# Performance work log

Hardware: AMD Instinct MI355X
Metric: run time of the kernel (lower is better)

## Reference

```python
import jax, jax.numpy as jnp
import numpy as np

N, E, R, F, HD = 4096, 2048, 4, 128, 256
DEG_EPS = 1e-8
BN_EPS = 1e-5
LN_EPS = 1e-5


def _xavier(k, shape):
    scale = np.sqrt(2.0 / (shape[-2] + shape[-1])).astype(np.float32)
    return jax.random.normal(k, shape, jnp.float32) * scale


def setup_inputs() -> dict:
    key = jax.random.key(0)
    ks = jax.random.split(key, 8)
    X = jax.random.normal(ks[0], (N, F), jnp.float32)
    # sparse binary incidence matrices, one per relation type, stacked [R,N,E]
    H = (jax.random.uniform(ks[1], (R, N, E)) < 0.05).astype(jnp.float32)
    return {
        "X": X,
        "H": H,
        "W1": _xavier(ks[2], (R, F, HD)),
        "W2": _xavier(ks[3], (R, HD, HD)),
        "W3": _xavier(ks[4], (R, HD, F)),
        "imp": jnp.ones((3, R), jnp.float32),        # relation_importance per conv layer
        "b1": jnp.zeros((HD,), jnp.float32),
        "b2": jnp.zeros((HD,), jnp.float32),
        "b3": jnp.zeros((F,), jnp.float32),
        "bn_gamma": jnp.ones((2, HD), jnp.float32),
        "bn_beta": jnp.zeros((2, HD), jnp.float32),
        "ln_gamma": jnp.ones((2, HD), jnp.float32),
        "ln_beta": jnp.zeros((2, HD), jnp.float32),
        "rel_attn": jnp.ones((R,), jnp.float32) / R,
    }


def typed_conv(X, Hw, W, imp, bias):
    # Hw: [R,N,E] weighted incidence; theta = Dv^{-1/2} H De^{-1/2} via row/col scaling
    dv = jnp.power(Hw.sum(axis=2) + DEG_EPS, -0.5)   # [R,N]
    de = jnp.power(Hw.sum(axis=1) + DEG_EPS, -0.5)   # [R,E]
    theta = Hw * dv[:, :, None] * de[:, None, :]     # [R,N,E]
    # (theta @ theta^T) @ X computed as theta @ (theta^T @ X) -- same math, no NxN
    t = jnp.einsum('rne,nf->ref', theta, X)          # [R,E,Fin]
    Hn = jnp.einsum('rne,ref->rnf', theta, t)        # [R,N,Fin]
    out = jnp.einsum('rnf,rfo->rno', Hn, W)          # [R,N,Fout]
    out = out * jax.nn.sigmoid(imp)[:, None, None]
    return out.sum(axis=0) + bias


def bn_ln_elu(X, bg, bb, lg, lb):
    # BatchNorm1d with batch statistics (biased var), then LayerNorm, then ELU
    mu = X.mean(axis=0)
    var = X.var(axis=0)
    X = (X - mu) * jax.lax.rsqrt(var + BN_EPS) * bg + bb
    m = X.mean(axis=-1, keepdims=True)
    v = X.var(axis=-1, keepdims=True)
    X = (X - m) * jax.lax.rsqrt(v + LN_EPS) * lg + lb
    return jax.nn.elu(X)


def reference(X, H, W1, W2, W3, imp, b1, b2, b3, bn_gamma, bn_beta, ln_gamma, ln_beta, rel_attn):
    rw = jax.nn.softmax(rel_attn)
    Hw = H * rw[:, None, None]                       # weighted incidence per relation
    h = typed_conv(X, Hw, W1, imp[0], b1)
    h = bn_ln_elu(h, bn_gamma[0], bn_beta[0], ln_gamma[0], ln_beta[0])
    h = typed_conv(h, Hw, W2, imp[1], b2)
    h = bn_ln_elu(h, bn_gamma[1], bn_beta[1], ln_gamma[1], ln_beta[1])
    out = typed_conv(h, Hw, W3, imp[2], b3)
    return out + X  # residual: out_channels == in_channels by construction
```

## Files before the change

kernel.cpp:

```cpp
#include <hip/hip_runtime.h>
#include <hip/hip_bf16.h>

#define NN 4096
#define EE 2048
#define RR 4
#define FF 128
#define HDD 256

typedef __attribute__((ext_vector_type(4))) float floatx4;
typedef __attribute__((ext_vector_type(8))) __bf16 bf16x8;

#define AS1 __attribute__((address_space(1)))
#define AS3 __attribute__((address_space(3)))

__device__ __forceinline__ void async16(const void* g, void* l) {
  __builtin_amdgcn_global_load_lds((const AS1 void*)(unsigned long long)(g),
                                   (AS3 void*)(unsigned int)(unsigned long long)(l),
                                   16, 0, 0);
}

__device__ inline unsigned short f2b(float x) {
  unsigned int u = __float_as_uint(x);
  unsigned int r = u + 0x7fffu + ((u >> 16) & 1u);
  return (unsigned short)(r >> 16);
}
__device__ inline float b2f(unsigned short u) { return __uint_as_float((unsigned int)u << 16); }

__device__ inline float rel_w(const float* rel, int r) {
  float m = fmaxf(fmaxf(rel[0], rel[1]), fmaxf(rel[2], rel[3]));
  float s = 0.f;
#pragma unroll
  for (int i = 0; i < RR; i++) s += expf(rel[i] - m);
  return expf(rel[r] - m) / s;
}

__global__ void k_prep1(const float* __restrict__ H, const float* __restrict__ rel,
                        const float* __restrict__ W1, const float* __restrict__ W2,
                        const float* __restrict__ W3, const float* __restrict__ imp,
                        float* __restrict__ dvs, unsigned long long* __restrict__ mask,
                        unsigned short* __restrict__ W1catT, unsigned short* __restrict__ W2T,
                        unsigned short* __restrict__ W3T, float* __restrict__ de, float* __restrict__ cs) {
  int b = blockIdx.x;
  if (b < 4096) {
    int wave = (b << 2) | (threadIdx.x >> 6);
    int lane = threadIdx.x & 63;
    int r = wave >> 12;
    const float* row = H + (size_t)wave * EE;
    unsigned long long* mrow = mask + (size_t)wave * (EE / 64);
    float s = 0.f;
    for (int j = 0; j < EE / 64; j++) {
      float h = row[j * 64 + lane];
      s += h;
      unsigned long long m = __ballot(h != 0.0f);
      if (lane == 0) mrow[j] = m;
    }
    for (int off = 32; off; off >>= 1) s += __shfl_down(s, off);
    if (lane == 0) {
      float rwr = rel_w(rel, r);
      dvs[wave] = rwr * rsqrtf(rwr * s + 1e-8f);
    }
  } else if (b < 4096 + 2048) {
    int idx = (b - 4096) * 256 + threadIdx.x;
    if (idx < RR * FF * HDD) {
      int o = idx % HDD, f = (idx / HDD) % FF, r = idx / (HDD * FF);
      float sg = 1.0f / (1.0f + expf(-imp[r]));
      W1catT[(size_t)o * (RR * FF) + r * FF + f] = f2b(sg * W1[((size_t)r * FF + f) * HDD + o]);
    } else if (idx < RR * FF * HDD + RR * HDD * HDD) {
      int j = idx - RR * FF * HDD;
      int c = j % HDD, o = (j / HDD) % HDD, r = j / (HDD * HDD);
      float sg = 1.0f / (1.0f + expf(-imp[RR + r]));
      W2T[j] = f2b(sg * W2[((size_t)r * HDD + c) * HDD + o]);
    } else {
      int j = idx - RR * FF * HDD - RR * HDD * HDD;
      int c = j % HDD, o = (j / HDD) % FF, r = j / (HDD * FF);
      float sg = 1.0f / (1.0f + expf(-imp[2 * RR + r]));
      W3T[j] = f2b(sg * W3[((size_t)r * HDD + c) * FF + o]);
    }
  } else {
    int i = (b - 6144) * 256 + threadIdx.x;
    if (i < RR * EE) de[i] = 0.f;
    else if (i < RR * EE + 2 * HDD) cs[i - RR * EE] = 0.f;
  }
}

__global__ void k_prep2(const unsigned long long* __restrict__ m1, unsigned long long* __restrict__ m2,
                        float* __restrict__ de, const float* __restrict__ X,
                        const float* __restrict__ dvs, unsigned short* __restrict__ XdvT) {
  __shared__ unsigned long long w[64 * 33];
  __shared__ unsigned short tile[64][65];
  int t = threadIdx.x;
  if (blockIdx.x < 256) {
    int r = blockIdx.x >> 6;
    int n0 = (blockIdx.x & 63) << 6;
    const unsigned long long* src = m1 + ((size_t)r * NN + n0) * 32;
#pragma unroll
    for (int i = 0; i < 8; i++) {
      int idx = t + i * 256;
      int n = idx >> 5, W = idx & 31;
      w[n * 33 + W] = src[idx];
    }
    __syncthreads();
    int wid = t >> 6, lane = t & 63;
    int v = n0 >> 6;
#pragma unroll
    for (int Wi = 0; Wi < 8; Wi++) {
      int W = wid * 8 + Wi;
      unsigned long long myw = w[lane * 33 + W];
      unsigned long long out = 0;
      for (int b = 0; b < 64; b++) {
        unsigned long long mm = __ballot(((myw >> b) & 1ULL) != 0);
        if (lane == b) out = mm;
      }
      m2[((size_t)r * EE + W * 64 + lane) * 64 + v] = out;
      atomicAdd(&de[r * EE + W * 64 + lane], (float)__popcll(out));
    }
  } else {
    int idx = blockIdx.x - 256;
    int c0 = (idx & 1) * 64, m0 = ((idx >> 1) & 63) * 64, r = idx >> 7;
    int tr = t >> 4, tc = t & 15;
#pragma unroll
    for (int i = 0; i < 4; i++) {
      int m = m0 + tr + 16 * i;
      float d = dvs[(size_t)r * NN + m];
      float4 v = *(const float4*)(X + (size_t)m * FF + c0 + tc * 4);
      tile[tr + 16 * i][tc * 4 + 0] = f2b(v.x * d);
      tile[tr + 16 * i][tc * 4 + 1] = f2b(v.y * d);
      tile[tr + 16 * i][tc * 4 + 2] = f2b(v.z * d);
      tile[tr + 16 * i][tc * 4 + 3] = f2b(v.w * d);
    }
    __syncthreads();
    unsigned short* db = XdvT + (size_t)r * FF * NN;
#pragma unroll
    for (int i = 0; i < 4; i++) {
      int c = c0 + tr + 16 * i;
      ushort4 v;
      v.x = tile[tc * 4 + 0][tr + 16 * i];
      v.y = tile[tc * 4 + 1][tr + 16 * i];
      v.z = tile[tc * 4 + 2][tr + 16 * i];
      v.w = tile[tc * 4 + 3][tr + 16 * i];
      *(ushort4*)(db + (size_t)c * NN + m0 + tc * 4) = v;
    }
  }
}

template <int DEC, int FLAT>
__global__ __launch_bounds__(256) void k_gemm3(
    const unsigned short* __restrict__ A, const unsigned short* __restrict__ BT,
    int K, int SK, int lda, int ldb, long a_rs, long b_rs,
    unsigned short* __restrict__ P, long c_ps, long c_rs, int ldc,
    const unsigned long long* __restrict__ dm, int dnw, long drow_rs,
    const float* __restrict__ dvs_,
    const float* __restrict__ cscale, long cs_rs,
    const float* __restrict__ derow, const float* __restrict__ decol,
    const float* __restrict__ rel) {
  __shared__ unsigned short Al[2][128 * 64];
  __shared__ unsigned short Bl[2][128 * 64];
  int tid = threadIdx.x, wid = tid >> 6, lane = tid & 63;
  int m0 = blockIdx.x << 7, n0 = blockIdx.y << 7;
  int z = blockIdx.z, zr = z / SK, kz = z - zr * SK;
  int Kc = K / SK;
  int r8 = lane >> 3, c8 = lane & 7;
  int swz = ((c8 ^ r8) << 3);
  const unsigned short* Ab = A + (DEC == 1 ? 0 : ((size_t)zr * a_rs + (size_t)m0 * lda + (size_t)kz * Kc));
  const unsigned short* Bb = BT + (DEC == 2 ? 0 : ((size_t)zr * b_rs + (size_t)n0 * ldb + (size_t)kz * Kc));
  const unsigned int* mrow = nullptr;
  int drow = 0, dhalf = 0, dsw = 0;
  unsigned long long dvpack = 0;
  if (DEC) {
    drow = tid >> 1; dhalf = tid & 1;
    dsw = drow & 7;
    if (FLAT) {
      int n = m0 + drow;
#pragma unroll
      for (int r4 = 0; r4 < 4; r4++)
        dvpack |= (unsigned long long)f2b(dvs_[(r4 << 12) + n]) << (r4 << 4);
    } else {
      long mrowOff = (long)zr * drow_rs + (DEC == 1 ? m0 : n0) + drow;
      mrow = (const unsigned int*)(dm + (size_t)mrowOff * dnw);
    }
  }
  auto stage = [&](int pb, int k0) {
    if (DEC != 1) {
#pragma unroll
      for (int t = 0; t < 4; t++) {
        int rbase = (wid << 5) + (t << 3);
        int row = rbase + r8;
        async16(Ab + (size_t)row * lda + k0 + swz, &Al[pb][rbase * 64 + lane * 8]);
      }
    }
    if (DEC != 2) {
#pragma unroll
      for (int t = 0; t < 4; t++) {
        int rbase = (wid << 5) + (t << 3);
        int row = rbase + r8;
        async16(Bb + (size_t)row * ldb + k0 + swz, &Bl[pb][rbase * 64 + lane * 8]);
      }
    }
    if (DEC) {
      unsigned short* Dl = (DEC == 1) ? &Al[pb][0] : &Bl[pb][0];
      long kglob = (long)kz * Kc + k0;
      unsigned int bits;
      unsigned short sval;
      if (FLAT) {
        int rr = (int)(kglob >> 11);
        int ew = (((int)kglob) & 2047) >> 5;
        bits = ((const unsigned int*)dm)[(((size_t)rr << 12) + (size_t)(m0 + drow)) * 64 + ew + dhalf];
        sval = (unsigned short)(dvpack >> ((rr & 3) << 4));
      } else {
        bits = mrow[(kglob >> 5) + dhalf];
        sval = (unsigned short)0x3F80;
      }
      uint4 zz = {0u, 0u, 0u, 0u};
#pragma unroll
      for (int g = 0; g < 4; g++) {
        int chunk = ((dhalf << 2) | g) ^ dsw;
        *(uint4*)&Dl[drow * 64 + chunk * 8] = zz;
      }
      while (bits) {
        int b = __builtin_ctz(bits);
        bits &= bits - 1;
        int kl = (dhalf << 5) + b;
        Dl[drow * 64 + (((kl >> 3) ^ dsw) << 3) + (kl & 7)] = sval;
      }
    }
  };
  int wm = (wid >> 1) << 6, wn = (wid & 1) << 6;
  int fm = lane & 15, quad = lane >> 4;
  int f7 = fm & 7;
  floatx4 acc[4][4];
#pragma unroll
  for (int i = 0; i < 4; i++)
#pragma unroll
    for (int j = 0; j < 4; j++) acc[i][j] = (floatx4){0.f, 0.f, 0.f, 0.f};
  auto compute = [&](int pb) {
#pragma unroll
    for (int ks = 0; ks < 2; ks++) {
      int kg = (ks << 2) | quad;
      int ko = ((kg ^ f7) << 3);
      bf16x8 a[4], b[4];
#pragma unroll
      for (int i = 0; i < 4; i++) {
        a[i] = *(const bf16x8*)&Al[pb][(wm + i * 16 + fm) * 64 + ko];
        b[i] = *(const bf16x8*)&Bl[pb][(wn + i * 16 + fm) * 64 + ko];
      }
#pragma unroll
      for (int i = 0; i < 4; i++)
#pragma unroll
        for (int j = 0; j < 4; j++)
          acc[i][j] = __builtin_amdgcn_mfma_f32_16x16x32_bf16(a[i], b[j], acc[i][j], 0, 0, 0);
    }
  };
  stage(0, 0);
  __syncthreads();
  for (int k0 = 0; k0 < Kc; k0 += 128) {
    if (k0 + 64 < Kc) stage(1, k0 + 64);
    compute(0);
    __syncthreads();
    if (k0 + 128 < Kc) stage(0, k0 + 128);
    compute(1);
    __syncthreads();
  }
  unsigned short* Cb = P + (size_t)kz * c_ps + (size_t)zr * c_rs;
  float rwr = (derow || decol) ? rel_w(rel, zr) : 0.f;
  float csc[4];
#pragma unroll
  for (int ni = 0; ni < 4; ni++) {
    int col = n0 + wn + ni * 16 + fm;
    float c = 1.0f;
    if (cscale) c = cscale[(size_t)zr * cs_rs + col];
    if (decol) c = 1.0f / (rwr * decol[(size_t)zr * EE + col] + 1e-8f);
    csc[ni] = c;
  }
#pragma unroll
  for (int mi = 0; mi < 4; mi++)
#pragma unroll
    for (int ni = 0; ni < 4; ni++)
#pragma unroll
      for (int v = 0; v < 4; v++) {
        int row = m0 + wm + mi * 16 + quad * 4 + v;
        int col = n0 + wn + ni * 16 + fm;
        float val = acc[mi][ni][v] * csc[ni];
        if (derow) val *= 1.0f / (rwr * derow[(size_t)zr * EE + row] + 1e-8f);
        Cb[(size_t)row * ldc + col] = f2b(val);
      }
}

__global__ void k_red_b(const unsigned short* __restrict__ P, unsigned short* __restrict__ out,
                        int SK, long region, float* __restrict__ cszero) {
  if (cszero && blockIdx.x == 0 && blockIdx.y == 0) {
    cszero[threadIdx.x] = 0.f;
    cszero[threadIdx.x + 256] = 0.f;
  }
  long i = ((long)blockIdx.x * 256 + threadIdx.x) * 8;
  int zr = blockIdx.y;
  const unsigned short* p = P + (size_t)zr * SK * region + i;
  float s[8] = {0, 0, 0, 0, 0, 0, 0, 0};
  for (int k = 0; k < SK; k++) {
    const unsigned short* q = p + (size_t)k * region;
    ushort4 a = *(const ushort4*)q;
    ushort4 b = *(const ushort4*)(q + 4);
    s[0] += b2f(a.x); s[1] += b2f(a.y); s[2] += b2f(a.z); s[3] += b2f(a.w);
    s[4] += b2f(b.x); s[5] += b2f(b.y); s[6] += b2f(b.z); s[7] += b2f(b.w);
  }
  ushort4 o0, o1;
  o0.x = f2b(s[0]); o0.y = f2b(s[1]); o0.z = f2b(s[2]); o0.w = f2b(s[3]);
  o1.x = f2b(s[4]); o1.y = f2b(s[5]); o1.z = f2b(s[6]); o1.w = f2b(s[7]);
  unsigned short* d = out + (size_t)zr * region + i;
  *(ushort4*)d = o0;
  *(ushort4*)(d + 4) = o1;
}

__global__ void k_redstats(const unsigned short* __restrict__ P, float* __restrict__ out,
                           float* __restrict__ cs, float* __restrict__ cs2, int Z) {
  __shared__ float sm[2][8][256];
  int cg = (threadIdx.x & 31) << 3;
  int rowt = threadIdx.x >> 5;
  int r0 = blockIdx.x * 32;
  float s[8] = {0, 0, 0, 0, 0, 0, 0, 0}, s2[8] = {0, 0, 0, 0, 0, 0, 0, 0};
  for (int j = 0; j < 4; j++) {
    int row = r0 + rowt * 4 + j;
    long idx = (long)row * HDD + cg;
    float acc[8] = {0, 0, 0, 0, 0, 0, 0, 0};
    for (int z = 0; z < Z; z++) {
      const unsigned short* p = P + (size_t)z * ((long)NN * HDD) + idx;
      ushort4 a = *(const ushort4*)p;
      ushort4 b = *(const ushort4*)(p + 4);
      acc[0] += b2f(a.x); acc[1] += b2f(a.y); acc[2] += b2f(a.z); acc[3] += b2f(a.w);
      acc[4] += b2f(b.x); acc[5] += b2f(b.y); acc[6] += b2f(b.z); acc[7] += b2f(b.w);
    }
    float4 o0 = {acc[0], acc[1], acc[2], acc[3]};
    float4 o1 = {acc[4], acc[5], acc[6], acc[7]};
    *(float4*)(out + idx) = o0;
    *(float4*)(out + idx + 4) = o1;
#pragma unroll
    for (int i = 0; i < 8; i++) { s[i] += acc[i]; s2[i] += acc[i] * acc[i]; }
  }
#pragma unroll
  for (int i = 0; i < 8; i++) { sm[0][rowt][cg + i] = s[i]; sm[1][rowt][cg + i] = s2[i]; }
  __syncthreads();
  int c = threadIdx.x;
  float a0 = 0, a1 = 0;
#pragma unroll
  for (int t = 0; t < 8; t++) { a0 += sm[0][t][c]; a1 += sm[1][t][c]; }
  atomicAdd(&cs[c], a0);
  atomicAdd(&cs2[c], a1);
}

__global__ void k_red_out(const unsigned short* __restrict__ P, const float* __restrict__ X,
                          const float* __restrict__ b3, float* __restrict__ out, int Z) {
  long i = ((long)blockIdx.x * 256 + threadIdx.x) * 4;
  int f = (int)(i & 127);
  float4 s = *(const float4*)(X + i);
  s.x += b3[f]; s.y += b3[f + 1]; s.z += b3[f + 2]; s.w += b3[f + 3];
  for (int z = 0; z < Z; z++) {
    ushort4 v = *(const ushort4*)(P + (size_t)z * (NN * FF) + i);
    s.x += b2f(v.x); s.y += b2f(v.y); s.z += b2f(v.z); s.w += b2f(v.w);
  }
  *(float4*)(out + i) = s;
}

__global__ void k_bnlnelu(const float* __restrict__ x, const float* __restrict__ cs, const float* __restrict__ cs2,
                          const float* __restrict__ bg, const float* __restrict__ bb,
                          const float* __restrict__ lg, const float* __restrict__ lb,
                          unsigned short* __restrict__ out) {
  int wid = threadIdx.x >> 6, lane = threadIdx.x & 63;
  int n = blockIdx.x * 4 + wid;
  float y[4];
  float m = 0.f;
#pragma unroll
  for (int j = 0; j < 4; j++) {
    int c = lane + 64 * j;
    float mu = cs[c] * (1.0f / NN);
    float var = cs2[c] * (1.0f / NN) - mu * mu;
    float xv = x[(size_t)n * HDD + c];
    y[j] = (xv - mu) * rsqrtf(var + 1e-5f) * bg[c] + bb[c];
    m += y[j];
  }
  for (int off = 32; off; off >>= 1) m += __shfl_down(m, off);
  m = __shfl(m, 0) * (1.0f / HDD);
  float var = 0.f;
#pragma unroll
  for (int j = 0; j < 4; j++) { float d = y[j] - m; var += d * d; }
  for (int off = 32; off; off >>= 1) var += __shfl_down(var, off);
  var = __shfl(var, 0) * (1.0f / HDD);
  float inv = rsqrtf(var + 1e-5f);
#pragma unroll
  for (int j = 0; j < 4; j++) {
    int c = lane + 64 * j;
    float z = (y[j] - m) * inv * lg[c] + lb[c];
    z = z > 0.f ? z : expm1f(z);
    out[(size_t)n * HDD + c] = f2b(z);
  }
}

extern "C" void kernel_launch(void* const* d_in, const int* in_sizes, int n_in,
                              void* d_out, int out_size, void* d_ws, size_t ws_size,
                              hipStream_t stream) {
  const float* X   = (const float*)d_in[0];
  const float* H   = (const float*)d_in[1];
  const float* W1  = (const float*)d_in[2];
  const float* W2  = (const float*)d_in[3];
  const float* W3  = (const float*)d_in[4];
  const float* imp = (const float*)d_in[5];
  const float* b3  = (const float*)d_in[8];
  const float* bng = (const float*)d_in[9];
  const float* bnb = (const float*)d_in[10];
  const float* lng = (const float*)d_in[11];
  const float* lnb = (const float*)d_in[12];
  const float* rel = (const float*)d_in[13];
  (void)in_sizes; (void)n_in; (void)out_size; (void)ws_size;

  char* w = (char*)d_ws;
  size_t off = 0;
  auto alloc = [&](size_t bytes) -> void* {
    void* p = w + off;
    off += (bytes + 255) & ~(size_t)255;
    return p;
  };
  float* dvs  = (float*)alloc((size_t)RR * NN * 4);
  float* de   = (float*)alloc((size_t)RR * EE * 4);
  float* cs   = (float*)alloc(2 * HDD * 4);
  unsigned long long* mask1 = (unsigned long long*)alloc((size_t)RR * NN * (EE / 64) * 8);
  unsigned long long* mask2 = (unsigned long long*)alloc((size_t)RR * EE * (NN / 64) * 8);
  unsigned short* bufP = (unsigned short*)alloc((size_t)16 * NN * HDD * 2);
  unsigned short* bufC = (unsigned short*)alloc((size_t)RR * EE * HDD * 2);
  unsigned short* bufD = (unsigned short*)alloc((size_t)RR * EE * HDD * 2);
  unsigned short* bufE = (unsigned short*)alloc((size_t)RR * EE * HDD * 2);
  float* convout = (float*)alloc((size_t)NN * HDD * 4);
  unsigned short* Xb    = (unsigned short*)alloc((size_t)NN * HDD * 2);
  unsigned short* XdvT  = (unsigned short*)alloc((size_t)RR * FF * NN * 2);
  unsigned short* hwdvT = (unsigned short*)alloc((size_t)RR * HDD * NN * 2);
  unsigned short* W1catT = (unsigned short*)alloc((size_t)RR * FF * HDD * 2);
  unsigned short* W2T    = (unsigned short*)alloc((size_t)RR * HDD * HDD * 2);
  unsigned short* W3T    = (unsigned short*)alloc((size_t)RR * HDD * FF * 2);
  unsigned short* Z1T  = bufD;
  unsigned short* bufE2 = bufE;
  unsigned short* ydvT = XdvT;
  unsigned short* bufC2 = bufC;

  k_prep1<<<4096 + 2048 + 34, 256, 0, stream>>>(H, rel, W1, W2, W3, imp,
                                                dvs, mask1, W1catT, W2T, W3T, de, cs);
  k_prep2<<<256 + 512, 256, 0, stream>>>(mask1, mask2, de, X, dvs, XdvT);

  k_gemm3<1, 0><<<dim3(EE / 128, 1, RR * 8), 256, 0, stream>>>(
      nullptr, XdvT, NN, 8, 0, NN, 0, (long)FF * NN,
      bufP, (long)EE * FF, 8L * EE * FF, FF,
      mask2, NN / 64, EE, nullptr, nullptr, 0, de, nullptr, rel);
  k_red_b<<<dim3((EE * FF) / 2048, RR), 256, 0, stream>>>(bufP, bufC, 8, (long)EE * FF, nullptr);
  k_gemm3<0, 0><<<dim3(HDD / 128, EE / 128, RR), 256, 0, stream>>>(
      W1catT, bufC, FF, 1, RR * FF, FF, FF, (long)EE * FF,
      Z1T, 0, EE, RR * EE,
      nullptr, 0, 0, nullptr, nullptr, 0, nullptr, nullptr, nullptr);
  k_gemm3<1, 1><<<dim3(NN / 128, HDD / 128, 8), 256, 0, stream>>>(
      nullptr, Z1T, RR * EE, 8, 0, RR * EE, 0, 0,
      bufP, (long)NN * HDD, 0, HDD,
      mask1, 0, 0, dvs, nullptr, 0, nullptr, nullptr, nullptr);
  k_redstats<<<NN / 32, 256, 0, stream>>>(bufP, convout, cs, cs + HDD, 8);
  k_bnlnelu<<<NN / 4, 256, 0, stream>>>(convout, cs, cs + HDD, bng, bnb, lng, lnb, Xb);

  k_gemm3<0, 0><<<dim3(HDD / 128, NN / 128, RR), 256, 0, stream>>>(
      W2T, Xb, HDD, 1, HDD, HDD, (long)HDD * HDD, 0,
      hwdvT, 0, (long)HDD * NN, NN,
      nullptr, 0, 0, nullptr, dvs, NN, nullptr, nullptr, nullptr);
  k_gemm3<2, 0><<<dim3(HDD / 128, EE / 128, RR * 4), 256, 0, stream>>>(
      hwdvT, nullptr, NN, 4, NN, 0, (long)HDD * NN, 0,
      bufP, (long)HDD * RR * EE, EE, RR * EE,
      mask2, NN / 64, EE, nullptr, nullptr, 0, nullptr, de, rel);
  k_red_b<<<dim3((HDD * RR * EE) / 2048, 1), 256, 0, stream>>>(
      bufP, bufE2, 4, (long)HDD * RR * EE, cs);
  k_gemm3<1, 1><<<dim3(NN / 128, HDD / 128, 8), 256, 0, stream>>>(
      nullptr, bufE2, RR * EE, 8, 0, RR * EE, 0, 0,
      bufP, (long)NN * HDD, 0, HDD,
      mask1, 0, 0, dvs, nullptr, 0, nullptr, nullptr, nullptr);
  k_redstats<<<NN / 32, 256, 0, stream>>>(bufP, convout, cs, cs + HDD, 8);
  k_bnlnelu<<<NN / 4, 256, 0, stream>>>(convout, cs, cs + HDD, bng + HDD, bnb + HDD, lng + HDD, lnb + HDD, Xb);

  k_gemm3<0, 0><<<dim3(1, NN / 128, RR), 256, 0, stream>>>(
      W3T, Xb, HDD, 1, HDD, HDD, (long)FF * HDD, 0,
      ydvT, 0, (long)FF * NN, NN,
      nullptr, 0, 0, nullptr, dvs, NN, nullptr, nullptr, nullptr);
  k_gemm3<2, 0><<<dim3(1, EE / 128, RR * 8), 256, 0, stream>>>(
      ydvT, nullptr, NN, 8, NN, 0, (long)FF * NN, 0,
      bufP, (long)FF * RR * EE, EE, RR * EE,
      mask2, NN / 64, EE, nullptr, nullptr, 0, nullptr, de, rel);
  k_red_b<<<dim3((FF * RR * EE) / 2048, 1), 256, 0, stream>>>(
      bufP, bufC2, 8, (long)FF * RR * EE, nullptr);
  k_gemm3<1, 1><<<dim3(NN / 128, 1, 16), 256, 0, stream>>>(
      nullptr, bufC2, RR * EE, 16, 0, RR * EE, 0, 0,
      bufP, (long)NN * FF, 0, FF,
      mask1, 0, 0, dvs, nullptr, 0, nullptr, nullptr, nullptr);
  k_red_out<<<(NN * FF) / 1024, 256, 0, stream>>>(bufP, X, b3, (float*)d_out, 16);
}
```

Baseline: 490.6 us.

## Replace dense decoded-mask GEMMs with bitmask sparse gather-sum kernels

Drops the dense GEMMs that expanded the binary incidence masks into bf16 tiles and multiplied them on the matrix cores. In their place come wave-per-row sparse kernels that walk the bitmask with readlane/ctz, gather rows of the transformed features, and accumulate them in fp32. This removes split-K partial buffers and their reduction kernels, and folds the degree scaling, the residual add and the output into the gather kernels. Feature layouts change from transposed to row-major to suit the gathers. At about 5% density this skips most of the zero work, but it trades dense MFMA throughput for irregular, latency-bound memory gathers with serial dependencies.

```diff
diff --git a/kernel.cpp b/kernel.cpp
--- a/kernel.cpp
+++ b/kernel.cpp
@@ -24,7 +24,6 @@
   unsigned int r = u + 0x7fffu + ((u >> 16) & 1u);
   return (unsigned short)(r >> 16);
 }
-__device__ inline float b2f(unsigned short u) { return __uint_as_float((unsigned int)u << 16); }
 
 __device__ inline float rel_w(const float* rel, int r) {
   float m = fmaxf(fmaxf(rel[0], rel[1]), fmaxf(rel[2], rel[3]));
@@ -39,7 +38,8 @@
                         const float* __restrict__ W3, const float* __restrict__ imp,
                         float* __restrict__ dvs, unsigned long long* __restrict__ mask,
                         unsigned short* __restrict__ W1catT, unsigned short* __restrict__ W2T,
-                        unsigned short* __restrict__ W3T, float* __restrict__ de, float* __restrict__ cs) {
+                        unsigned short* __restrict__ W3T, float* __restrict__ de,
+                        float* __restrict__ csbuf) {
   int b = blockIdx.x;
   if (b < 4096) {
     int wave = (b << 2) | (threadIdx.x >> 6);
@@ -79,15 +79,14 @@
   } else {
     int i = (b - 6144) * 256 + threadIdx.x;
     if (i < RR * EE) de[i] = 0.f;
-    else if (i < RR * EE + 2 * HDD) cs[i - RR * EE] = 0.f;
+    else if (i < RR * EE + 8 * 512) csbuf[i - RR * EE] = 0.f;
   }
 }
 
 __global__ void k_prep2(const unsigned long long* __restrict__ m1, unsigned long long* __restrict__ m2,
                         float* __restrict__ de, const float* __restrict__ X,
-                        const float* __restrict__ dvs, unsigned short* __restrict__ XdvT) {
+                        const float* __restrict__ dvs, unsigned short* __restrict__ Xdv) {
   __shared__ unsigned long long w[64 * 33];
-  __shared__ unsigned short tile[64][65];
   int t = threadIdx.x;
   if (blockIdx.x < 256) {
     int r = blockIdx.x >> 6;
@@ -115,113 +114,42 @@
       atomicAdd(&de[r * EE + W * 64 + lane], (float)__popcll(out));
     }
   } else {
-    int idx = blockIdx.x - 256;
-    int c0 = (idx & 1) * 64, m0 = ((idx >> 1) & 63) * 64, r = idx >> 7;
-    int tr = t >> 4, tc = t & 15;
-#pragma unroll
-    for (int i = 0; i < 4; i++) {
-      int m = m0 + tr + 16 * i;
-      float d = dvs[(size_t)r * NN + m];
-      float4 v = *(const float4*)(X + (size_t)m * FF + c0 + tc * 4);
-      tile[tr + 16 * i][tc * 4 + 0] = f2b(v.x * d);
-      tile[tr + 16 * i][tc * 4 + 1] = f2b(v.y * d);
-      tile[tr + 16 * i][tc * 4 + 2] = f2b(v.z * d);
-      tile[tr + 16 * i][tc * 4 + 3] = f2b(v.w * d);
-    }
-    __syncthreads();
-    unsigned short* db = XdvT + (size_t)r * FF * NN;
-#pragma unroll
-    for (int i = 0; i < 4; i++) {
-      int c = c0 + tr + 16 * i;
-      ushort4 v;
-      v.x = tile[tc * 4 + 0][tr + 16 * i];
-      v.y = tile[tc * 4 + 1][tr + 16 * i];
-      v.z = tile[tc * 4 + 2][tr + 16 * i];
-      v.w = tile[tc * 4 + 3][tr + 16 * i];
-      *(ushort4*)(db + (size_t)c * NN + m0 + tc * 4) = v;
-    }
-  }
-}
-
-template <int DEC, int FLAT>
+    int g = (blockIdx.x - 256) * 256 + t;
+    int f8 = g & 15, n = (g >> 4) & (NN - 1), r = g >> 16;
+    const float* xp = X + (size_t)n * FF + (f8 << 3);
+    float4 v0 = *(const float4*)xp;
+    float4 v1 = *(const float4*)(xp + 4);
+    float d = dvs[(r << 12) + n];
+    ushort4 o0, o1;
+    o0.x = f2b(v0.x * d); o0.y = f2b(v0.y * d); o0.z = f2b(v0.z * d); o0.w = f2b(v0.w * d);
+    o1.x = f2b(v1.x * d); o1.y = f2b(v1.y * d); o1.z = f2b(v1.z * d); o1.w = f2b(v1.w * d);
+    unsigned short* dp = Xdv + ((size_t)r * NN + n) * FF + (f8 << 3);
+    *(ushort4*)dp = o0;
+    *(ushort4*)(dp + 4) = o1;
+  }
+}
+
 __global__ __launch_bounds__(256) void k_gemm3(
     const unsigned short* __restrict__ A, const unsigned short* __restrict__ BT,
-    int K, int SK, int lda, int ldb, long a_rs, long b_rs,
-    unsigned short* __restrict__ P, long c_ps, long c_rs, int ldc,
-    const unsigned long long* __restrict__ dm, int dnw, long drow_rs,
-    const float* __restrict__ dvs_,
-    const float* __restrict__ cscale, long cs_rs,
-    const float* __restrict__ derow, const float* __restrict__ decol,
-    const float* __restrict__ rel) {
+    int K, int lda, int ldb, long a_rs, long b_rs,
+    unsigned short* __restrict__ P, long c_rs, int ldc,
+    const float* __restrict__ rscale, long rs_rs) {
   __shared__ unsigned short Al[2][128 * 64];
   __shared__ unsigned short Bl[2][128 * 64];
   int tid = threadIdx.x, wid = tid >> 6, lane = tid & 63;
   int m0 = blockIdx.x << 7, n0 = blockIdx.y << 7;
-  int z = blockIdx.z, zr = z / SK, kz = z - zr * SK;
-  int Kc = K / SK;
+  int zr = blockIdx.z;
   int r8 = lane >> 3, c8 = lane & 7;
   int swz = ((c8 ^ r8) << 3);
-  const unsigned short* Ab = A + (DEC == 1 ? 0 : ((size_t)zr * a_rs + (size_t)m0 * lda + (size_t)kz * Kc));
-  const unsigned short* Bb = BT + (DEC == 2 ? 0 : ((size_t)zr * b_rs + (size_t)n0 * ldb + (size_t)kz * Kc));
-  const unsigned int* mrow = nullptr;
-  int drow = 0, dhalf = 0, dsw = 0;
-  unsigned long long dvpack = 0;
-  if (DEC) {
-    drow = tid >> 1; dhalf = tid & 1;
-    dsw = drow & 7;
-    if (FLAT) {
-      int n = m0 + drow;
-#pragma unroll
-      for (int r4 = 0; r4 < 4; r4++)
-        dvpack |= (unsigned long long)f2b(dvs_[(r4 << 12) + n]) << (r4 << 4);
-    } else {
-      long mrowOff = (long)zr * drow_rs + (DEC == 1 ? m0 : n0) + drow;
-      mrow = (const unsigned int*)(dm + (size_t)mrowOff * dnw);
-    }
-  }
+  const unsigned short* Ab = A + (size_t)zr * a_rs + (size_t)m0 * lda;
+  const unsigned short* Bb = BT + (size_t)zr * b_rs + (size_t)n0 * ldb;
   auto stage = [&](int pb, int k0) {
-    if (DEC != 1) {
-#pragma unroll
-      for (int t = 0; t < 4; t++) {
-        int rbase = (wid << 5) + (t << 3);
-        int row = rbase + r8;
-        async16(Ab + (size_t)row * lda + k0 + swz, &Al[pb][rbase * 64 + lane * 8]);
-      }
-    }
-    if (DEC != 2) {
-#pragma unroll
-      for (int t = 0; t < 4; t++) {
-        int rbase = (wid << 5) + (t << 3);
-        int row = rbase + r8;
-        async16(Bb + (size_t)row * ldb + k0 + swz, &Bl[pb][rbase * 64 + lane * 8]);
-      }
-    }
-    if (DEC) {
-      unsigned short* Dl = (DEC == 1) ? &Al[pb][0] : &Bl[pb][0];
-      long kglob = (long)kz * Kc + k0;
-      unsigned int bits;
-      unsigned short sval;
-      if (FLAT) {
-        int rr = (int)(kglob >> 11);
-        int ew = (((int)kglob) & 2047) >> 5;
-        bits = ((const unsigned int*)dm)[(((size_t)rr << 12) + (size_t)(m0 + drow)) * 64 + ew + dhalf];
-        sval = (unsigned short)(dvpack >> ((rr & 3) << 4));
-      } else {
-        bits = mrow[(kglob >> 5) + dhalf];
-        sval = (unsigned short)0x3F80;
-      }
-      uint4 zz = {0u, 0u, 0u, 0u};
-#pragma unroll
-      for (int g = 0; g < 4; g++) {
-        int chunk = ((dhalf << 2) | g) ^ dsw;
-        *(uint4*)&Dl[drow * 64 + chunk * 8] = zz;
-      }
-      while (bits) {
-        int b = __builtin_ctz(bits);
-        bits &= bits - 1;
-        int kl = (dhalf << 5) + b;
-        Dl[drow * 64 + (((kl >> 3) ^ dsw) << 3) + (kl & 7)] = sval;
-      }
+#pragma unroll
+    for (int t = 0; t < 4; t++) {
+      int rbase = (wid << 5) + (t << 3);
+      int row = rbase + r8;
+      async16(Ab + (size_t)row * lda + k0 + swz, &Al[pb][rbase * 64 + lane * 8]);
+      async16(Bb + (size_t)row * ldb + k0 + swz, &Bl[pb][rbase * 64 + lane * 8]);
     }
   };
   int wm = (wid >> 1) << 6, wn = (wid & 1) << 6;
@@ -252,114 +180,236 @@
   };
   stage(0, 0);
   __syncthreads();
-  for (int k0 = 0; k0 < Kc; k0 += 128) {
-    if (k0 + 64 < Kc) stage(1, k0 + 64);
+  for (int k0 = 0; k0 < K; k0 += 128) {
+    if (k0 + 64 < K) stage(1, k0 + 64);
     compute(0);
     __syncthreads();
-    if (k0 + 128 < Kc) stage(0, k0 + 128);
+    if (k0 + 128 < K) stage(0, k0 + 128);
     compute(1);
     __syncthreads();
   }
-  unsigned short* Cb = P + (size_t)kz * c_ps + (size_t)zr * c_rs;
-  float rwr = (derow || decol) ? rel_w(rel, zr) : 0.f;
-  float csc[4];
-#pragma unroll
-  for (int ni = 0; ni < 4; ni++) {
-    int col = n0 + wn + ni * 16 + fm;
-    float c = 1.0f;
-    if (cscale) c = cscale[(size_t)zr * cs_rs + col];
-    if (decol) c = 1.0f / (rwr * decol[(size_t)zr * EE + col] + 1e-8f);
-    csc[ni] = c;
-  }
+  unsigned short* Cb = P + (size_t)zr * c_rs;
 #pragma unroll
   for (int mi = 0; mi < 4; mi++)
 #pragma unroll
-    for (int ni = 0; ni < 4; ni++)
-#pragma unroll
-      for (int v = 0; v < 4; v++) {
-        int row = m0 + wm + mi * 16 + quad * 4 + v;
+    for (int v = 0; v < 4; v++) {
+      int row = m0 + wm + mi * 16 + quad * 4 + v;
+      float rs = rscale ? rscale[(size_t)zr * rs_rs + row] : 1.0f;
+#pragma unroll
+      for (int ni = 0; ni < 4; ni++) {
         int col = n0 + wn + ni * 16 + fm;
-        float val = acc[mi][ni][v] * csc[ni];
-        if (derow) val *= 1.0f / (rwr * derow[(size_t)zr * EE + row] + 1e-8f);
-        Cb[(size_t)row * ldc + col] = f2b(val);
-      }
-}
-
-__global__ void k_red_b(const unsigned short* __restrict__ P, unsigned short* __restrict__ out,
-                        int SK, long region, float* __restrict__ cszero) {
-  if (cszero && blockIdx.x == 0 && blockIdx.y == 0) {
-    cszero[threadIdx.x] = 0.f;
-    cszero[threadIdx.x + 256] = 0.f;
-  }
-  long i = ((long)blockIdx.x * 256 + threadIdx.x) * 8;
-  int zr = blockIdx.y;
-  const unsigned short* p = P + (size_t)zr * SK * region + i;
-  float s[8] = {0, 0, 0, 0, 0, 0, 0, 0};
-  for (int k = 0; k < SK; k++) {
-    const unsigned short* q = p + (size_t)k * region;
-    ushort4 a = *(const ushort4*)q;
-    ushort4 b = *(const ushort4*)(q + 4);
-    s[0] += b2f(a.x); s[1] += b2f(a.y); s[2] += b2f(a.z); s[3] += b2f(a.w);
-    s[4] += b2f(b.x); s[5] += b2f(b.y); s[6] += b2f(b.z); s[7] += b2f(b.w);
-  }
-  ushort4 o0, o1;
-  o0.x = f2b(s[0]); o0.y = f2b(s[1]); o0.z = f2b(s[2]); o0.w = f2b(s[3]);
-  o1.x = f2b(s[4]); o1.y = f2b(s[5]); o1.z = f2b(s[6]); o1.w = f2b(s[7]);
-  unsigned short* d = out + (size_t)zr * region + i;
-  *(ushort4*)d = o0;
-  *(ushort4*)(d + 4) = o1;
-}
-
-__global__ void k_redstats(const unsigned short* __restrict__ P, float* __restrict__ out,
-                           float* __restrict__ cs, float* __restrict__ cs2, int Z) {
-  __shared__ float sm[2][8][256];
-  int cg = (threadIdx.x & 31) << 3;
-  int rowt = threadIdx.x >> 5;
-  int r0 = blockIdx.x * 32;
-  float s[8] = {0, 0, 0, 0, 0, 0, 0, 0}, s2[8] = {0, 0, 0, 0, 0, 0, 0, 0};
-  for (int j = 0; j < 4; j++) {
-    int row = r0 + rowt * 4 + j;
-    long idx = (long)row * HDD + cg;
-    float acc[8] = {0, 0, 0, 0, 0, 0, 0, 0};
-    for (int z = 0; z < Z; z++) {
-      const unsigned short* p = P + (size_t)z * ((long)NN * HDD) + idx;
-      ushort4 a = *(const ushort4*)p;
-      ushort4 b = *(const ushort4*)(p + 4);
-      acc[0] += b2f(a.x); acc[1] += b2f(a.y); acc[2] += b2f(a.z); acc[3] += b2f(a.w);
-      acc[4] += b2f(b.x); acc[5] += b2f(b.y); acc[6] += b2f(b.z); acc[7] += b2f(b.w);
-    }
-    float4 o0 = {acc[0], acc[1], acc[2], acc[3]};
-    float4 o1 = {acc[4], acc[5], acc[6], acc[7]};
-    *(float4*)(out + idx) = o0;
-    *(float4*)(out + idx + 4) = o1;
-#pragma unroll
-    for (int i = 0; i < 8; i++) { s[i] += acc[i]; s2[i] += acc[i] * acc[i]; }
-  }
-#pragma unroll
-  for (int i = 0; i < 8; i++) { sm[0][rowt][cg + i] = s[i]; sm[1][rowt][cg + i] = s2[i]; }
+        Cb[(size_t)row * ldc + col] = f2b(acc[mi][ni][v] * rs);
+      }
+    }
+}
+
+template <int C>
+__global__ __launch_bounds__(256) void k_b2s(
+    const unsigned long long* __restrict__ mask2, const unsigned short* __restrict__ T,
+    const float* __restrict__ de, const float* __restrict__ rel,
+    unsigned short* __restrict__ out, float* __restrict__ csz) {
+  if (blockIdx.x == 0) {
+#pragma unroll
+    for (int i = 0; i < 16; i++) csz[i * 256 + threadIdx.x] = 0.f;
+  }
+  int wv = (blockIdx.x << 2) | (threadIdx.x >> 6);
+  int lane = threadIdx.x & 63;
+  int r = wv >> 11, e = wv & (EE - 1);
+  unsigned long long w = mask2[(size_t)wv * 64 + lane];
+  unsigned int wlo = (unsigned int)w, whi = (unsigned int)(w >> 32);
+  const unsigned short* Tr = T + (size_t)r * NN * C;
+  float a0 = 0.f, a1 = 0.f, a2 = 0.f, a3 = 0.f;
+  int v = 0;
+  unsigned long long bits = 0;
+  while (v < 64 && bits == 0) {
+    unsigned int lo = (unsigned int)__builtin_amdgcn_readlane((int)wlo, v);
+    unsigned int hi = (unsigned int)__builtin_amdgcn_readlane((int)whi, v);
+    bits = ((unsigned long long)hi << 32) | lo;
+    v++;
+  }
+  bool have = bits != 0;
+  unsigned int u0 = 0, u1 = 0;
+  if (have) {
+    int b = __builtin_ctzll(bits);
+    bits &= bits - 1;
+    const unsigned short* rp = Tr + (size_t)(((v - 1) << 6) + b) * C;
+    if (C == 256) { uint2 uu = *(const uint2*)(rp + (lane << 2)); u0 = uu.x; u1 = uu.y; }
+    else u0 = *(const unsigned int*)(rp + (lane << 1));
+  }
+  while (have) {
+    while (v < 64 && bits == 0) {
+      unsigned int lo = (unsigned int)__builtin_amdgcn_readlane((int)wlo, v);
+      unsigned int hi = (unsigned int)__builtin_amdgcn_readlane((int)whi, v);
+      bits = ((unsigned long long)hi << 32) | lo;
+      v++;
+    }
+    bool haven = bits != 0;
+    unsigned int n0 = 0, n1 = 0;
+    if (haven) {
+      int b = __builtin_ctzll(bits);
+      bits &= bits - 1;
+      const unsigned short* rp = Tr + (size_t)(((v - 1) << 6) + b) * C;
+      if (C == 256) { uint2 uu = *(const uint2*)(rp + (lane << 2)); n0 = uu.x; n1 = uu.y; }
+      else n0 = *(const unsigned int*)(rp + (lane << 1));
+    }
+    a0 += __uint_as_float(u0 << 16);
+    a1 += __uint_as_float(u0 & 0xffff0000u);
+    if (C == 256) {
+      a2 += __uint_as_float(u1 << 16);
+      a3 += __uint_as_float(u1 & 0xffff0000u);
+    }
+    u0 = n0; u1 = n1; have = haven;
+  }
+  float rwr = rel_w(rel, r);
+  float s = 1.0f / (rwr * de[(r << 11) + e] + 1e-8f);
+  unsigned short* op = out + (size_t)wv * C;
+  if (C == 256) {
+    ushort4 o;
+    o.x = f2b(a0 * s); o.y = f2b(a1 * s); o.z = f2b(a2 * s); o.w = f2b(a3 * s);
+    *(ushort4*)(op + (lane << 2)) = o;
+  } else {
+    ushort2 o;
+    o.x = f2b(a0 * s); o.y = f2b(a1 * s);
+    *(ushort2*)(op + (lane << 1)) = o;
+  }
+}
+
+__global__ __launch_bounds__(256) void k_b1s256(
+    const unsigned long long* __restrict__ mask1, const unsigned short* __restrict__ T,
+    const float* __restrict__ dvs, float* __restrict__ out, float* __restrict__ csbuf) {
+  __shared__ float sm[4][256];
+  int wid = threadIdx.x >> 6, lane = threadIdx.x & 63;
+  int n = (blockIdx.x << 1) | (wid >> 1);
+  int rh = wid & 1;
+  float y0 = 0.f, y1 = 0.f, y2 = 0.f, y3 = 0.f;
+#pragma unroll
+  for (int rr = 0; rr < 2; rr++) {
+    int r = (rh << 1) | rr;
+    unsigned long long w = mask1[((size_t)(r << 12) + n) * 32 + (lane & 31)];
+    unsigned int wlo = (unsigned int)w, whi = (unsigned int)(w >> 32);
+    const unsigned short* Tr = T + (size_t)r * EE * 256;
+    float a0 = 0.f, a1 = 0.f, a2 = 0.f, a3 = 0.f;
+    int v = 0;
+    unsigned long long bits = 0;
+    while (v < 32 && bits == 0) {
+      unsigned int lo = (unsigned int)__builtin_amdgcn_readlane((int)wlo, v);
+      unsigned int hi = (unsigned int)__builtin_amdgcn_readlane((int)whi, v);
+      bits = ((unsigned long long)hi << 32) | lo;
+      v++;
+    }
+    bool have = bits != 0;
+    unsigned int u0 = 0, u1 = 0;
+    if (have) {
+      int b = __builtin_ctzll(bits);
+      bits &= bits - 1;
+      const unsigned short* rp = Tr + (size_t)(((v - 1) << 6) + b) * 256;
+      uint2 uu = *(const uint2*)(rp + (lane << 2));
+      u0 = uu.x; u1 = uu.y;
+    }
+    while (have) {
+      while (v < 32 && bits == 0) {
+        unsigned int lo = (unsigned int)__builtin_amdgcn_readlane((int)wlo, v);
+        unsigned int hi = (unsigned int)__builtin_amdgcn_readlane((int)whi, v);
+        bits = ((unsigned long long)hi << 32) | lo;
+        v++;
+      }
+      bool haven = bits != 0;
+      unsigned int p0 = 0, p1 = 0;
+      if (haven) {
+        int b = __builtin_ctzll(bits);
+        bits &= bits - 1;
+        const unsigned short* rp = Tr + (size_t)(((v - 1) << 6) + b) * 256;
+        uint2 uu = *(const uint2*)(rp + (lane << 2));
+        p0 = uu.x; p1 = uu.y;
+      }
+      a0 += __uint_as_float(u0 << 16);
+      a1 += __uint_as_float(u0 & 0xffff0000u);
+      a2 += __uint_as_float(u1 << 16);
+      a3 += __uint_as_float(u1 & 0xffff0000u);
+      u0 = p0; u1 = p1; have = haven;
+    }
+    float dv = dvs[(r << 12) + n];
+    y0 += dv * a0; y1 += dv * a1; y2 += dv * a2; y3 += dv * a3;
+  }
+  float4 yv = {y0, y1, y2, y3};
+  *(float4*)&sm[wid][lane << 2] = yv;
   __syncthreads();
   int c = threadIdx.x;
-  float a0 = 0, a1 = 0;
-#pragma unroll
-  for (int t = 0; t < 8; t++) { a0 += sm[0][t][c]; a1 += sm[1][t][c]; }
-  atomicAdd(&cs[c], a0);
-  atomicAdd(&cs2[c], a1);
-}
-
-__global__ void k_red_out(const unsigned short* __restrict__ P, const float* __restrict__ X,
-                          const float* __restrict__ b3, float* __restrict__ out, int Z) {
-  long i = ((long)blockIdx.x * 256 + threadIdx.x) * 4;
-  int f = (int)(i & 127);
-  float4 s = *(const float4*)(X + i);
-  s.x += b3[f]; s.y += b3[f + 1]; s.z += b3[f + 2]; s.w += b3[f + 3];
-  for (int z = 0; z < Z; z++) {
-    ushort4 v = *(const ushort4*)(P + (size_t)z * (NN * FF) + i);
-    s.x += b2f(v.x); s.y += b2f(v.y); s.z += b2f(v.z); s.w += b2f(v.w);
-  }
-  *(float4*)(out + i) = s;
-}
-
-__global__ void k_bnlnelu(const float* __restrict__ x, const float* __restrict__ cs, const float* __restrict__ cs2,
+  float ya = sm[0][c] + sm[1][c];
+  float yb = sm[2][c] + sm[3][c];
+  int n0 = blockIdx.x << 1;
+  out[(size_t)n0 * HDD + c] = ya;
+  out[(size_t)(n0 + 1) * HDD + c] = yb;
+  float* csb = csbuf + ((blockIdx.x & 7) << 9);
+  atomicAdd(&csb[c], ya + yb);
+  atomicAdd(&csb[c + 256], ya * ya + yb * yb);
+}
+
+__global__ __launch_bounds__(256) void k_b1s128o(
+    const unsigned long long* __restrict__ mask1, const unsigned short* __restrict__ T,
+    const float* __restrict__ dvs, const float* __restrict__ X, const float* __restrict__ b3,
+    float* __restrict__ out) {
+  __shared__ float sm[4][128];
+  int wid = threadIdx.x >> 6, lane = threadIdx.x & 63;
+  int n = (blockIdx.x << 1) | (wid >> 1);
+  int rh = wid & 1;
+  float y0 = 0.f, y1 = 0.f;
+#pragma unroll
+  for (int rr = 0; rr < 2; rr++) {
+    int r = (rh << 1) | rr;
+    unsigned long long w = mask1[((size_t)(r << 12) + n) * 32 + (lane & 31)];
+    unsigned int wlo = (unsigned int)w, whi = (unsigned int)(w >> 32);
+    const unsigned short* Tr = T + (size_t)r * EE * 128;
+    float a0 = 0.f, a1 = 0.f;
+    int v = 0;
+    unsigned long long bits = 0;
+    while (v < 32 && bits == 0) {
+      unsigned int lo = (unsigned int)__builtin_amdgcn_readlane((int)wlo, v);
+      unsigned int hi = (unsigned int)__builtin_amdgcn_readlane((int)whi, v);
+      bits = ((unsigned long long)hi << 32) | lo;
+      v++;
+    }
+    bool have = bits != 0;
+    unsigned int u0 = 0;
+    if (have) {
+      int b = __builtin_ctzll(bits);
+      bits &= bits - 1;
+      const unsigned short* rp = Tr + (size_t)(((v - 1) << 6) + b) * 128;
+      u0 = *(const unsigned int*)(rp + (lane << 1));
+    }
+    while (have) {
+      while (v < 32 && bits == 0) {
+        unsigned int lo = (unsigned int)__builtin_amdgcn_readlane((int)wlo, v);
+        unsigned int hi = (unsigned int)__builtin_amdgcn_readlane((int)whi, v);
+        bits = ((unsigned long long)hi << 32) | lo;
+        v++;
+      }
+      bool haven = bits != 0;
+      unsigned int p0 = 0;
+      if (haven) {
+        int b = __builtin_ctzll(bits);
+        bits &= bits - 1;
+        const unsigned short* rp = Tr + (size_t)(((v - 1) << 6) + b) * 128;
+        p0 = *(const unsigned int*)(rp + (lane << 1));
+      }
+      a0 += __uint_as_float(u0 << 16);
+      a1 += __uint_as_float(u0 & 0xffff0000u);
+      u0 = p0; have = haven;
+    }
+    float dv = dvs[(r << 12) + n];
+    y0 += dv * a0; y1 += dv * a1;
+  }
+  float2 yv = {y0, y1};
+  *(float2*)&sm[wid][lane << 1] = yv;
+  __syncthreads();
+  int t = threadIdx.x;
+  int c = t & 127, nl = t >> 7;
+  int nn = (blockIdx.x << 1) + nl;
+  float y = sm[nl * 2][c] + sm[nl * 2 + 1][c];
+  out[(size_t)nn * FF + c] = X[(size_t)nn * FF + c] + b3[c] + y;
+}
+
+__global__ void k_bnlnelu(const float* __restrict__ x, const float* __restrict__ csbuf,
                           const float* __restrict__ bg, const float* __restrict__ bb,
                           const float* __restrict__ lg, const float* __restrict__ lb,
                           unsigned short* __restrict__ out) {
@@ -370,8 +420,14 @@
 #pragma unroll
   for (int j = 0; j < 4; j++) {
     int c = lane + 64 * j;
-    float mu = cs[c] * (1.0f / NN);
-    float var = cs2[c] * (1.0f / NN) - mu * mu;
+    float s0 = 0.f, s1 = 0.f;
+#pragma unroll
+    for (int k = 0; k < 8; k++) {
+      s0 += csbuf[k * 512 + c];
+      s1 += csbuf[k * 512 + 256 + c];
+    }
+    float mu = s0 * (1.0f / NN);
+    float var = s1 * (1.0f / NN) - mu * mu;
     float xv = x[(size_t)n * HDD + c];
     y[j] = (xv - mu) * rsqrtf(var + 1e-5f) * bg[c] + bb[c];
     m += y[j];
@@ -417,77 +473,42 @@
     off += (bytes + 255) & ~(size_t)255;
     return p;
   };
-  float* dvs  = (float*)alloc((size_t)RR * NN * 4);
-  float* de   = (float*)alloc((size_t)RR * EE * 4);
-  float* cs   = (float*)alloc(2 * HDD * 4);
-  unsigned long long* mask1 = (unsigned long long*)alloc((size_t)RR * NN * (EE / 64) * 8);
-  unsigned long long* mask2 = (unsigned long long*)alloc((size_t)RR * EE * (NN / 64) * 8);
-  unsigned short* bufP = (unsigned short*)alloc((size_t)16 * NN * HDD * 2);
-  unsigned short* bufC = (unsigned short*)alloc((size_t)RR * EE * HDD * 2);
-  unsigned short* bufD = (unsigned short*)alloc((size_t)RR * EE * HDD * 2);
-  unsigned short* bufE = (unsigned short*)alloc((size_t)RR * EE * HDD * 2);
-  float* convout = (float*)alloc((size_t)NN * HDD * 4);
-  unsigned short* Xb    = (unsigned short*)alloc((size_t)NN * HDD * 2);
-  unsigned short* XdvT  = (unsigned short*)alloc((size_t)RR * FF * NN * 2);
-  unsigned short* hwdvT = (unsigned short*)alloc((size_t)RR * HDD * NN * 2);
+  float* dvs   = (float*)alloc((size_t)RR * NN * 4);
+  float* de    = (float*)alloc((size_t)RR * EE * 4);
+  float* csbuf = (float*)alloc(8 * 512 * 4);
+  unsigned long long* mask1 = (unsigned long long*)alloc((size_t)RR * NN * 32 * 8);
+  unsigned long long* mask2 = (unsigned long long*)alloc((size_t)RR * EE * 64 * 8);
+  unsigned short* Xdv  = (unsigned short*)alloc((size_t)RR * NN * FF * 2);
+  unsigned short* t1   = (unsigned short*)alloc((size_t)RR * EE * FF * 2);
+  unsigned short* Z1   = (unsigned short*)alloc((size_t)RR * EE * HDD * 2);
+  float* convout       = (float*)alloc((size_t)NN * HDD * 4);
+  unsigned short* Xb   = (unsigned short*)alloc((size_t)NN * HDD * 2);
+  unsigned short* hwdv = (unsigned short*)alloc((size_t)RR * NN * HDD * 2);
+  unsigned short* t2   = (unsigned short*)alloc((size_t)RR * EE * HDD * 2);
+  unsigned short* ydv  = (unsigned short*)alloc((size_t)RR * NN * FF * 2);
+  unsigned short* t3   = (unsigned short*)alloc((size_t)RR * EE * FF * 2);
   unsigned short* W1catT = (unsigned short*)alloc((size_t)RR * FF * HDD * 2);
   unsigned short* W2T    = (unsigned short*)alloc((size_t)RR * HDD * HDD * 2);
   unsigned short* W3T    = (unsigned short*)alloc((size_t)RR * HDD * FF * 2);
-  unsigned short* Z1T  = bufD;
-  unsigned short* bufE2 = bufE;
-  unsigned short* ydvT = XdvT;
-  unsigned short* bufC2 = bufC;
-
-  k_prep1<<<4096 + 2048 + 34, 256, 0, stream>>>(H, rel, W1, W2, W3, imp,
-                                                dvs, mask1, W1catT, W2T, W3T, de, cs);
-  k_prep2<<<256 + 512, 256, 0, stream>>>(mask1, mask2, de, X, dvs, XdvT);
-
-  k_gemm3<1, 0><<<dim3(EE / 128, 1, RR * 8), 256, 0, stream>>>(
-      nullptr, XdvT, NN, 8, 0, NN, 0, (long)FF * NN,
-      bufP, (long)EE * FF, 8L * EE * FF, FF,
-      mask2, NN / 64, EE, nullptr, nullptr, 0, de, nullptr, rel);
-  k_red_b<<<dim3((EE * FF) / 2048, RR), 256, 0, stream>>>(bufP, bufC, 8, (long)EE * FF, nullptr);
-  k_gemm3<0, 0><<<dim3(HDD / 128, EE / 128, RR), 256, 0, stream>>>(
-      W1catT, bufC, FF, 1, RR * FF, FF, FF, (long)EE * FF,
-      Z1T, 0, EE, RR * EE,
-      nullptr, 0, 0, nullptr, nullptr, 0, nullptr, nullptr, nullptr);
-  k_gemm3<1, 1><<<dim3(NN / 128, HDD / 128, 8), 256, 0, stream>>>(
-      nullptr, Z1T, RR * EE, 8, 0, RR * EE, 0, 0,
-      bufP, (long)NN * HDD, 0, HDD,
-      mask1, 0, 0, dvs, nullptr, 0, nullptr, nullptr, nullptr);
-  k_redstats<<<NN / 32, 256, 0, stream>>>(bufP, convout, cs, cs + HDD, 8);
-  k_bnlnelu<<<NN / 4, 256, 0, stream>>>(convout, cs, cs + HDD, bng, bnb, lng, lnb, Xb);
-
-  k_gemm3<0, 0><<<dim3(HDD / 128, NN / 128, RR), 256, 0, stream>>>(
-      W2T, Xb, HDD, 1, HDD, HDD, (long)HDD * HDD, 0,
-      hwdvT, 0, (long)HDD * NN, NN,
-      nullptr, 0, 0, nullptr, dvs, NN, nullptr, nullptr, nullptr);
-  k_gemm3<2, 0><<<dim3(HDD / 128, EE / 128, RR * 4), 256, 0, stream>>>(
-      hwdvT, nullptr, NN, 4, NN, 0, (long)HDD * NN, 0,
-      bufP, (long)HDD * RR * EE, EE, RR * EE,
-      mask2, NN / 64, EE, nullptr, nullptr, 0, nullptr, de, rel);
-  k_red_b<<<dim3((HDD * RR * EE) / 2048, 1), 256, 0, stream>>>(
-      bufP, bufE2, 4, (long)HDD * RR * EE, cs);
-  k_gemm3<1, 1><<<dim3(NN / 128, HDD / 128, 8), 256, 0, stream>>>(
-      nullptr, bufE2, RR * EE, 8, 0, RR * EE, 0, 0,
-      bufP, (long)NN * HDD, 0, HDD,
-      mask1, 0, 0, dvs, nullptr, 0, nullptr, nullptr, nullptr);
-  k_redstats<<<NN / 32, 256, 0, stream>>>(bufP, convout, cs, cs + HDD, 8);
-  k_bnlnelu<<<NN / 4, 256, 0, stream>>>(convout, cs, cs + HDD, bng + HDD, bnb + HDD, lng + HDD, lnb + HDD, Xb);
-
-  k_gemm3<0, 0><<<dim3(1, NN / 128, RR), 256, 0, stream>>>(
-      W3T, Xb, HDD, 1, HDD, HDD, (long)FF * HDD, 0,
-      ydvT, 0, (long)FF * NN, NN,
-      nullptr, 0, 0, nullptr, dvs, NN, nullptr, nullptr, nullptr);
-  k_gemm3<2, 0><<<dim3(1, EE / 128, RR * 8), 256, 0, stream>>>(
-      ydvT, nullptr, NN, 8, NN, 0, (long)FF * NN, 0,
-      bufP, (long)FF * RR * EE, EE, RR * EE,
-      mask2, NN / 64, EE, nullptr, nullptr, 0, nullptr, de, rel);
-  k_red_b<<<dim3((FF * RR * EE) / 2048, 1), 256, 0, stream>>>(
-      bufP, bufC2, 8, (long)FF * RR * EE, nullptr);
-  k_gemm3<1, 1><<<dim3(NN / 128, 1, 16), 256, 0, stream>>>(
-      nullptr, bufC2, RR * EE, 16, 0, RR * EE, 0, 0,
-      bufP, (long)NN * FF, 0, FF,
-      mask1, 0, 0, dvs, nullptr, 0, nullptr, nullptr, nullptr);
-  k_red_out<<<(NN * FF) / 1024, 256, 0, stream>>>(bufP, X, b3, (float*)d_out, 16);
-}
+
+  k_prep1<<<4096 + 2048 + 48, 256, 0, stream>>>(H, rel, W1, W2, W3, imp,
+                                                dvs, mask1, W1catT, W2T, W3T, de, csbuf);
+  k_prep2<<<256 + 1024, 256, 0, stream>>>(mask1, mask2, de, X, dvs, Xdv);
+
+  k_b2s<128><<<2048, 256, 0, stream>>>(mask2, Xdv, de, rel, t1, csbuf);
+  k_gemm3<<<dim3(EE / 128, HDD / 128, RR), 256, 0, stream>>>(
+      t1, W1catT, FF, FF, RR * FF, (long)EE * FF, FF, Z1, (long)EE * HDD, HDD, nullptr, 0);
+  k_b1s256<<<NN / 2, 256, 0, stream>>>(mask1, Z1, dvs, convout, csbuf);
+  k_bnlnelu<<<NN / 4, 256, 0, stream>>>(convout, csbuf, bng, bnb, lng, lnb, Xb);
+
+  k_gemm3<<<dim3(NN / 128, HDD / 128, RR), 256, 0, stream>>>(
+      Xb, W2T, HDD, HDD, HDD, 0, (long)HDD * HDD, hwdv, (long)NN * HDD, HDD, dvs, NN);
+  k_b2s<256><<<2048, 256, 0, stream>>>(mask2, hwdv, de, rel, t2, csbuf);
+  k_b1s256<<<NN / 2, 256, 0, stream>>>(mask1, t2, dvs, convout, csbuf);
+  k_bnlnelu<<<NN / 4, 256, 0, stream>>>(convout, csbuf, bng + HDD, bnb + HDD, lng + HDD, lnb + HDD, Xb);
+
+  k_gemm3<<<dim3(NN / 128, 1, RR), 256, 0, stream>>>(
+      Xb, W3T, HDD, HDD, HDD, 0, (long)FF * HDD, ydv, (long)NN * FF, FF, dvs, NN);
+  k_b2s<128><<<2048, 256, 0, stream>>>(mask2, ydv, de, rel, t3, csbuf);
+  k_b1s128o<<<NN / 2, 256, 0, stream>>>(mask1, t3, dvs, X, b3, (float*)d_out);
+}
```

After: 870.3 us. +77.4%, slower.
